# Kernel tuning notes

Hardware: AMD Instinct MI355X
Metric: run time of the kernel (lower is better)

## Reference

```python
import jax, jax.numpy as jnp
import numpy as np

N_GRP = 2048   # n groups
L = 64         # kv slots per group
Q = 4096       # total queries (nq.sum())
D = 256        # d_q = d_k = d_h
DZ = 256       # attention projection dim d_z
DX = 256       # token embedding dim
NTYP = 64      # relation types
NTOK = 50000   # token vocab
M = 131072     # memory tokens
G = 16384      # scatter_sum groups
B = 1024       # examples for scatter_min


def setup_inputs() -> dict:
    key = jax.random.key(0)
    ks = jax.random.split(key, 16)
    q = jax.random.normal(ks[0], (Q, D), jnp.float32)
    k = jax.random.normal(ks[1], (N_GRP, L, D), jnp.float32)
    m = jax.random.bernoulli(ks[2], 0.7, (N_GRP, L))
    m = m.at[:, 0].set(True)  # guarantee >=1 valid slot per group
    # per-query group index == repeat_interleave(arange(n), nq) with nq = 2
    qgrp = jnp.repeat(jnp.arange(N_GRP, dtype=jnp.int32), Q // N_GRP)
    mem = jax.random.randint(ks[3], (M,), 0, NTOK, jnp.int32)
    grp = jnp.sort(jax.random.randint(ks[4], (M,), 0, G, jnp.int32))
    pos2grp = jax.random.randint(ks[5], (N_GRP, L), 0, G, jnp.int32)
    typ = jax.random.randint(ks[6], (Q, NTYP), 0, 2, jnp.int32).astype(bool)
    idx = jnp.sort(jax.random.randint(ks[7], (Q,), 0, B, jnp.int32))
    s = lambda d: 1.0 / np.sqrt(d).astype(np.float32)
    emb = jax.random.normal(ks[8], (NTOK, DX), jnp.float32)
    Wq = jax.random.normal(ks[9], (DZ, D), jnp.float32) * s(D)
    bq = jnp.zeros((DZ,), jnp.float32)
    Wk = jax.random.normal(ks[10], (DZ, D), jnp.float32) * s(D)
    bk = jnp.zeros((DZ,), jnp.float32)
    Wrel = jax.random.normal(ks[11], (NTYP, D + DX), jnp.float32) * s(D + DX)
    brel = jnp.zeros((NTYP,), jnp.float32)
    return dict(q=q, k=k, emb=emb, Wq=Wq, bq=bq, Wk=Wk, bk=bk, Wrel=Wrel,
                brel=brel, m=m, qgrp=qgrp, mem=mem, grp=grp, pos2grp=pos2grp,
                typ=typ, idx=idx)


def reference(q, k, emb, Wq, bq, Wk, bk, Wrel, brel, m, qgrp, mem, grp,
              pos2grp, typ, idx):
    # x_all = scatter_sum(tok_embedding(mem), grp, 0)[pos2grp] : (n, l, dx)
    x_all = jax.ops.segment_sum(emb[mem], grp, num_segments=G)[pos2grp]
    # Attention (ragged masked softmax over l, per-query group gather)
    qz = q @ Wq.T + bq                      # (Q, dz)
    kz = k @ Wk.T + bk                      # (n, l, dz)
    s = jnp.einsum('qd,qld->ql', qz, kz[qgrp]) / np.sqrt(DZ).astype(np.float32)
    s = jnp.where(m[qgrp], s, -jnp.inf)     # masked_fill(~m, -inf)
    p = jax.nn.softmax(s, axis=1)           # softmax over l
    att = jnp.einsum('ql,qld->qd', p, x_all[qgrp])   # (Q, dx)
    logit = jnp.concatenate([q, att], axis=-1) @ Wrel.T + brel  # (Q, n_typ)
    gt = logit > 0
    eq = gt == typ
    acc = eq.astype(jnp.float32).mean()
    em = jax.ops.segment_min(eq.all(1).astype(jnp.int32), idx, num_segments=B)
    emr = em.astype(jnp.float32).mean()
    # binary_cross_entropy_with_logits, reduction='sum', / len(m)
    nll = (jnp.logaddexp(0.0, logit) - logit * typ.astype(logit.dtype)).sum() / N_GRP
    return (logit, acc, emr, nll, em)
```

## Files before the change

kernel.cpp:

```cpp
#include <hip/hip_runtime.h>
#include <hip/hip_bf16.h>
#include <math.h>

#define N_GRP 2048
#define LSLOT 64
#define NQ    4096
#define DIM   256
#define NTYPE 64
#define MMEM  131072
#define GSEG  16384
#define BEX   1024

#define OFF_SEG   0u
#define OFF_QW    4194304u
#define OFF_MT    5242880u
#define OFF_VB    5308416u
#define OFF_WB    5308672u
#define OFF_SB    5308928u
#define OFF_EM    5308936u
#define OFF_CNT   5309960u
#define OFF_NLL   5309964u
#define OFF_FLAG  5309966u

#define OUT_ACC 262144
#define OUT_EMR 262145
#define OUT_NLL 262146
#define OUT_EM  262147

__device__ __forceinline__ bool rd_bool(const void* p, int i, int mode) {
  if (mode == 0) return ((const int*)p)[i] != 0;
  if (mode == 1) return ((const unsigned char*)p)[i] != 0;
  return ((const float*)p)[i] != 0.f;
}

__global__ __launch_bounds__(256)
void k_pre(const float* __restrict__ Wq, const float* __restrict__ bq,
           const float* __restrict__ Wk, const float* __restrict__ bk,
           const void* __restrict__ typ, float* __restrict__ ws) {
  int b = blockIdx.x, t = threadIdx.x;
  if (b < 32) {
    int j0 = b * 8;
    float acc[8] = {0.f,0.f,0.f,0.f,0.f,0.f,0.f,0.f};
    for (int z = 0; z < 256; ++z) {
      float wk = Wk[z * 256 + t];
      const float* wq = Wq + z * 256 + j0;
      #pragma unroll
      for (int u = 0; u < 8; ++u) acc[u] += wq[u] * wk;
    }
    #pragma unroll
    for (int u = 0; u < 8; ++u) ws[OFF_MT + (unsigned)(j0 + u) * 256 + t] = acc[u];
  } else if (b == 32) {
    float a = 0.f;
    for (int z = 0; z < 256; ++z) a += Wq[z * 256 + t] * bk[z];
    ws[OFF_VB + t] = a;
  } else if (b == 33) {
    float a = 0.f;
    for (int z = 0; z < 256; ++z) a += Wk[z * 256 + t] * bq[z];
    ws[OFF_WB + t] = a;
    __shared__ float red[256];
    red[t] = bq[t] * bk[t];
    __syncthreads();
    for (int st = 128; st; st >>= 1) { if (t < st) red[t] += red[t + st]; __syncthreads(); }
    if (t == 0) ws[OFF_SB] = red[0];
  } else {
    __shared__ int fl_f, fl_b;
    if (t == 0) { fl_f = 0; fl_b = 0; }
    __syncthreads();
    for (int i = t; i < 4096; i += 256) {
      unsigned wv = ((const unsigned*)typ)[i];
      if (wv == 0x3F800000u) atomicOr(&fl_f, 1);
      else if (wv > 1u)      atomicOr(&fl_b, 1);
    }
    __syncthreads();
    int* em = (int*)(ws + OFF_EM);
    for (int i = t; i < BEX; i += 256) em[i] = 0x7FFFFFFF;
    if (t == 0) {
      *(int*)(ws + OFF_FLAG) = fl_f ? 2 : (fl_b ? 1 : 0);
      *(int*)(ws + OFF_CNT) = 0;
      *(double*)(ws + OFF_NLL) = 0.0;
    }
  }
}

__global__ __launch_bounds__(256)
void k_seg(const float* __restrict__ emb, const int* __restrict__ mem,
           const int* __restrict__ grp, float* __restrict__ ws) {
  int t = threadIdx.x;
  int lane = t & 63, w = t >> 6;
  int g = blockIdx.x * 4 + w;
  int lo = 0, hi = MMEM;
  while (lo < hi) { int mid = (lo + hi) >> 1; if (grp[mid] < g) lo = mid + 1; else hi = mid; }
  int lo2 = lo, hi2 = MMEM;
  while (lo2 < hi2) { int mid = (lo2 + hi2) >> 1; if (grp[mid] < g + 1) lo2 = mid + 1; else hi2 = mid; }
  float4 acc = {0.f, 0.f, 0.f, 0.f};
  for (int r = lo; r < lo2; ++r) {
    int tok = mem[r];
    float4 v = *(const float4*)(emb + (size_t)tok * 256 + lane * 4);
    acc.x += v.x; acc.y += v.y; acc.z += v.z; acc.w += v.w;
  }
  *(float4*)(ws + OFF_SEG + (size_t)g * 256 + lane * 4) = acc;
}

__global__ __launch_bounds__(256)
void k_qw(const float* __restrict__ q, float* __restrict__ ws) {
  int b = blockIdx.x, t = threadIdx.x;
  int r0 = b * 16;
  const float* MT = ws + OFF_MT;
  float acc[16];
  float wbv = ws[OFF_WB + t];
  #pragma unroll
  for (int r = 0; r < 16; ++r) acc[r] = wbv;
  for (int j = 0; j < 256; j += 4) {
    float m0 = MT[(j + 0) * 256 + t];
    float m1 = MT[(j + 1) * 256 + t];
    float m2 = MT[(j + 2) * 256 + t];
    float m3 = MT[(j + 3) * 256 + t];
    #pragma unroll
    for (int r = 0; r < 16; ++r) {
      float4 q4 = *(const float4*)(q + (size_t)(r0 + r) * 256 + j);
      acc[r] += q4.x * m0 + q4.y * m1 + q4.z * m2 + q4.w * m3;
    }
  }
  #pragma unroll
  for (int r = 0; r < 16; ++r) ws[OFF_QW + (unsigned)(r0 + r) * 256 + t] = acc[r];
}

__global__ __launch_bounds__(256)
void k_attn(const float* __restrict__ q, const float* __restrict__ k,
            const float* __restrict__ Wrel, const float* __restrict__ brel,
            const void* __restrict__ mmask, const int* __restrict__ pos2grp,
            const void* __restrict__ typ, const int* __restrict__ idx,
            float* __restrict__ ws, float* __restrict__ out) {
  int g = blockIdx.x;
  int t = threadIdx.x;
  int lane = t & 63, w = t >> 6;
  __shared__ float qw_l[2][256], qr_l[2][256], att_l[2][256];
  __shared__ float s_l[2][64], p_l[2][64];
  __shared__ float att_p[4][2][64][4];
  __shared__ float cq_l[2];
  __shared__ float nll_l;
  __shared__ int eqcnt_l, all_l[2];
  const int q0 = 2 * g;
  const int mode = *(const int*)(ws + OFF_FLAG);

  qw_l[0][t] = ws[OFF_QW + (unsigned)q0 * 256 + t];
  qw_l[1][t] = ws[OFF_QW + (unsigned)(q0 + 1) * 256 + t];
  qr_l[0][t] = q[(size_t)q0 * 256 + t];
  qr_l[1][t] = q[(size_t)(q0 + 1) * 256 + t];
  if (t == 0) { eqcnt_l = 0; nll_l = 0.f; all_l[0] = 1; all_l[1] = 1; }
  if (w < 2) {
    const float* qrow = q + (size_t)(q0 + w) * 256;
    float p = 0.f;
    #pragma unroll
    for (int u = 0; u < 4; ++u) p += qrow[lane + 64 * u] * ws[OFF_VB + lane + 64 * u];
    for (int off = 32; off; off >>= 1) p += __shfl_xor(p, off);
    if (lane == 0) cq_l[w] = p + ws[OFF_SB];
  }
  __syncthreads();

  const float* kg = k + (size_t)g * LSLOT * 256;
  for (int li = 0; li < 16; ++li) {
    int l = w * 16 + li;
    bool valid = rd_bool(mmask, g * LSLOT + l, mode);
    if (!valid) {
      if (lane == 0) { s_l[0][l] = -INFINITY; s_l[1][l] = -INFINITY; }
      continue;
    }
    float4 kv = *(const float4*)(kg + l * 256 + lane * 4);
    float4 w0 = *(const float4*)&qw_l[0][lane * 4];
    float4 w1 = *(const float4*)&qw_l[1][lane * 4];
    float s0 = kv.x * w0.x + kv.y * w0.y + kv.z * w0.z + kv.w * w0.w;
    float s1 = kv.x * w1.x + kv.y * w1.y + kv.z * w1.z + kv.w * w1.w;
    for (int off = 32; off; off >>= 1) { s0 += __shfl_xor(s0, off); s1 += __shfl_xor(s1, off); }
    if (lane == 0) {
      s_l[0][l] = (s0 + cq_l[0]) * 0.0625f;
      s_l[1][l] = (s1 + cq_l[1]) * 0.0625f;
    }
  }
  __syncthreads();

  if (w < 2) {
    float v = s_l[w][lane];
    float mx = v;
    for (int off = 32; off; off >>= 1) mx = fmaxf(mx, __shfl_xor(mx, off));
    float e = expf(v - mx);
    float ssum = e;
    for (int off = 32; off; off >>= 1) ssum += __shfl_xor(ssum, off);
    p_l[w][lane] = e / ssum;
  }
  __syncthreads();

  {
    float4 a0 = {0.f,0.f,0.f,0.f}, a1 = {0.f,0.f,0.f,0.f};
    const float* seg = ws + OFF_SEG;
    const int* pg = pos2grp + g * LSLOT;
    for (int li = 0; li < 16; ++li) {
      int l = li * 4 + w;
      float p0 = p_l[0][l], p1 = p_l[1][l];
      if (p0 == 0.f && p1 == 0.f) continue;
      int row = pg[l];
      float4 v = *(const float4*)(seg + (size_t)row * 256 + lane * 4);
      a0.x += p0 * v.x; a0.y += p0 * v.y; a0.z += p0 * v.z; a0.w += p0 * v.w;
      a1.x += p1 * v.x; a1.y += p1 * v.y; a1.z += p1 * v.z; a1.w += p1 * v.w;
    }
    *(float4*)&att_p[w][0][lane][0] = a0;
    *(float4*)&att_p[w][1][lane][0] = a1;
  }
  __syncthreads();
  {
    int dl = t >> 2, dc = t & 3;
    #pragma unroll
    for (int qi = 0; qi < 2; ++qi)
      att_l[qi][t] = att_p[0][qi][dl][dc] + att_p[1][qi][dl][dc]
                   + att_p[2][qi][dl][dc] + att_p[3][qi][dl][dc];
  }
  __syncthreads();

  {
    int cnt = 0, allf = 1;
    float nllp = 0.f;
    int qi = w >> 1;
    int tbase = (w & 1) * 32;
    const float* src = (lane < 32) ? &qr_l[qi][lane * 8] : &att_l[qi][(lane - 32) * 8];
    float4 xa = *(const float4*)src;
    float4 xb = *(const float4*)(src + 4);
    for (int it = 0; it < 32; ++it) {
      int tt = tbase + it;
      const float* wr = Wrel + tt * 512 + lane * 8;
      float4 wa = *(const float4*)wr;
      float4 wb4 = *(const float4*)(wr + 4);
      float d = xa.x * wa.x + xa.y * wa.y + xa.z * wa.z + xa.w * wa.w
              + xb.x * wb4.x + xb.y * wb4.y + xb.z * wb4.z + xb.w * wb4.w;
      for (int off = 32; off; off >>= 1) d += __shfl_xor(d, off);
      if (lane == 0) {
        float lg = d + brel[tt];
        out[(size_t)(q0 + qi) * NTYPE + tt] = lg;
        bool gt = lg > 0.f;
        bool tv = rd_bool(typ, (q0 + qi) * NTYPE + tt, mode);
        bool eqv = (gt == tv);
        cnt += (int)eqv;
        allf &= (int)eqv;
        nllp += fmaxf(lg, 0.f) + log1pf(expf(-fabsf(lg))) - (tv ? lg : 0.f);
      }
    }
    if (lane == 0) {
      atomicAdd(&eqcnt_l, cnt);
      atomicAnd(&all_l[qi], allf);
      atomicAdd(&nll_l, nllp);
    }
  }
  __syncthreads();
  if (t == 0) {
    atomicAdd((int*)(ws + OFF_CNT), eqcnt_l);
    atomicAdd((double*)(ws + OFF_NLL), (double)nll_l);
    int* em = (int*)(ws + OFF_EM);
    atomicMin(&em[idx[q0]], all_l[0]);
    atomicMin(&em[idx[q0 + 1]], all_l[1]);
  }
}

__global__ __launch_bounds__(256)
void k_fin(float* __restrict__ ws, float* __restrict__ out) {
  __shared__ float red[256];
  int t = threadIdx.x;
  const int* em = (const int*)(ws + OFF_EM);
  float s = 0.f;
  for (int i = t; i < BEX; i += 256) {
    float v = (float)em[i];
    out[OUT_EM + i] = v;
    s += v;
  }
  red[t] = s; __syncthreads();
  for (int st = 128; st; st >>= 1) { if (t < st) red[t] += red[t + st]; __syncthreads(); }
  if (t == 0) {
    out[OUT_ACC] = (float)(*(const int*)(ws + OFF_CNT)) / (float)(NQ * NTYPE);
    out[OUT_EMR] = red[0] / (float)BEX;
    out[OUT_NLL] = (float)((*(const double*)(ws + OFF_NLL)) / (double)N_GRP);
  }
}

extern "C" void kernel_launch(void* const* d_in, const int* in_sizes, int n_in,
                              void* d_out, int out_size, void* d_ws, size_t ws_size,
                              hipStream_t stream) {
  const float* q    = (const float*)d_in[0];
  const float* k    = (const float*)d_in[1];
  const float* emb  = (const float*)d_in[2];
  const float* Wq   = (const float*)d_in[3];
  const float* bq   = (const float*)d_in[4];
  const float* Wk   = (const float*)d_in[5];
  const float* bk   = (const float*)d_in[6];
  const float* Wrel = (const float*)d_in[7];
  const float* brel = (const float*)d_in[8];
  const void* mmask   = d_in[9];
  const int* mem      = (const int*)d_in[11];
  const int* grp      = (const int*)d_in[12];
  const int* pos2grp  = (const int*)d_in[13];
  const void* typ     = d_in[14];
  const int* idx      = (const int*)d_in[15];
  float* ws  = (float*)d_ws;
  float* out = (float*)d_out;

  k_pre <<<35,     256, 0, stream>>>(Wq, bq, Wk, bk, typ, ws);
  k_seg <<<GSEG/4, 256, 0, stream>>>(emb, mem, grp, ws);
  k_qw  <<<NQ/16,  256, 0, stream>>>(q, ws);
  k_attn<<<N_GRP,  256, 0, stream>>>(q, k, Wrel, brel, mmask, pos2grp, typ, idx, ws, out);
  k_fin <<<1,      256, 0, stream>>>(ws, out);
}
```

Measured before the change: 467.1 us.

## Merge segment-sum and query projection kernels, restructure attention dot products

Spreads the Wq·Wk precompute over 256 blocks instead of 32. Fuses the segment-sum and q·M kernels into one launch and removes a launch boundary. In the segment-sum, tokens are loaded once per wave and broadcast by shuffle, with four embedding rows fetched per iteration for more memory-level parallelism. In the attention kernel, the score and Wrel dot products now use 4-lane partial sums with short shuffle reductions instead of full 64-lane reductions, and masking is moved into the softmax. The logit epilogue uses a wave ballot. The combined kernel mixes two very different block workloads, and k loads are no longer skipped for masked slots.

```diff
diff --git a/kernel.cpp b/kernel.cpp
--- a/kernel.cpp
+++ b/kernel.cpp
@@ -38,23 +38,21 @@
            const float* __restrict__ Wk, const float* __restrict__ bk,
            const void* __restrict__ typ, float* __restrict__ ws) {
   int b = blockIdx.x, t = threadIdx.x;
-  if (b < 32) {
-    int j0 = b * 8;
-    float acc[8] = {0.f,0.f,0.f,0.f,0.f,0.f,0.f,0.f};
-    for (int z = 0; z < 256; ++z) {
-      float wk = Wk[z * 256 + t];
-      const float* wq = Wq + z * 256 + j0;
-      #pragma unroll
-      for (int u = 0; u < 8; ++u) acc[u] += wq[u] * wk;
-    }
-    #pragma unroll
-    for (int u = 0; u < 8; ++u) ws[OFF_MT + (unsigned)(j0 + u) * 256 + t] = acc[u];
-  } else if (b == 32) {
+  if (b < 256) {
+    int j = b;
+    float acc = 0.f;
+    #pragma unroll 8
+    for (int z = 0; z < 256; ++z)
+      acc += Wk[z * 256 + t] * Wq[z * 256 + j];
+    ws[OFF_MT + (unsigned)j * 256 + t] = acc;
+  } else if (b == 256) {
     float a = 0.f;
+    #pragma unroll 8
     for (int z = 0; z < 256; ++z) a += Wq[z * 256 + t] * bk[z];
     ws[OFF_VB + t] = a;
-  } else if (b == 33) {
+  } else if (b == 257) {
     float a = 0.f;
+    #pragma unroll 8
     for (int z = 0; z < 256; ++z) a += Wk[z * 256 + t] * bq[z];
     ws[OFF_WB + t] = a;
     __shared__ float red[256];
@@ -83,46 +81,67 @@
 }
 
 __global__ __launch_bounds__(256)
-void k_seg(const float* __restrict__ emb, const int* __restrict__ mem,
-           const int* __restrict__ grp, float* __restrict__ ws) {
+void k_segqw(const float* __restrict__ emb, const int* __restrict__ mem,
+             const int* __restrict__ grp, const float* __restrict__ q,
+             float* __restrict__ ws) {
   int t = threadIdx.x;
-  int lane = t & 63, w = t >> 6;
-  int g = blockIdx.x * 4 + w;
-  int lo = 0, hi = MMEM;
-  while (lo < hi) { int mid = (lo + hi) >> 1; if (grp[mid] < g) lo = mid + 1; else hi = mid; }
-  int lo2 = lo, hi2 = MMEM;
-  while (lo2 < hi2) { int mid = (lo2 + hi2) >> 1; if (grp[mid] < g + 1) lo2 = mid + 1; else hi2 = mid; }
-  float4 acc = {0.f, 0.f, 0.f, 0.f};
-  for (int r = lo; r < lo2; ++r) {
-    int tok = mem[r];
-    float4 v = *(const float4*)(emb + (size_t)tok * 256 + lane * 4);
-    acc.x += v.x; acc.y += v.y; acc.z += v.z; acc.w += v.w;
-  }
-  *(float4*)(ws + OFF_SEG + (size_t)g * 256 + lane * 4) = acc;
-}
-
-__global__ __launch_bounds__(256)
-void k_qw(const float* __restrict__ q, float* __restrict__ ws) {
-  int b = blockIdx.x, t = threadIdx.x;
-  int r0 = b * 16;
-  const float* MT = ws + OFF_MT;
-  float acc[16];
-  float wbv = ws[OFF_WB + t];
-  #pragma unroll
-  for (int r = 0; r < 16; ++r) acc[r] = wbv;
-  for (int j = 0; j < 256; j += 4) {
-    float m0 = MT[(j + 0) * 256 + t];
-    float m1 = MT[(j + 1) * 256 + t];
-    float m2 = MT[(j + 2) * 256 + t];
-    float m3 = MT[(j + 3) * 256 + t];
-    #pragma unroll
-    for (int r = 0; r < 16; ++r) {
-      float4 q4 = *(const float4*)(q + (size_t)(r0 + r) * 256 + j);
-      acc[r] += q4.x * m0 + q4.y * m1 + q4.z * m2 + q4.w * m3;
-    }
-  }
-  #pragma unroll
-  for (int r = 0; r < 16; ++r) ws[OFF_QW + (unsigned)(r0 + r) * 256 + t] = acc[r];
+  if (blockIdx.x < GSEG / 4) {
+    int lane = t & 63, w = t >> 6;
+    int g = blockIdx.x * 4 + w;
+    int lo = 0, hi = MMEM;
+    while (lo < hi) { int mid = (lo + hi) >> 1; if (grp[mid] < g) lo = mid + 1; else hi = mid; }
+    int lo2 = lo, hi2 = MMEM;
+    while (lo2 < hi2) { int mid = (lo2 + hi2) >> 1; if (grp[mid] < g + 1) lo2 = mid + 1; else hi2 = mid; }
+    int n = lo2 - lo;
+    int nv = n < 64 ? n : 64;
+    int tok = (lane < nv) ? mem[lo + lane] : 0;
+    float4 acc = {0.f, 0.f, 0.f, 0.f};
+    int r = 0;
+    for (; r + 4 <= nv; r += 4) {
+      int t0 = __shfl(tok, r + 0), t1 = __shfl(tok, r + 1);
+      int t2 = __shfl(tok, r + 2), t3 = __shfl(tok, r + 3);
+      float4 v0 = *(const float4*)(emb + (size_t)t0 * 256 + lane * 4);
+      float4 v1 = *(const float4*)(emb + (size_t)t1 * 256 + lane * 4);
+      float4 v2 = *(const float4*)(emb + (size_t)t2 * 256 + lane * 4);
+      float4 v3 = *(const float4*)(emb + (size_t)t3 * 256 + lane * 4);
+      acc.x += (v0.x + v1.x) + (v2.x + v3.x);
+      acc.y += (v0.y + v1.y) + (v2.y + v3.y);
+      acc.z += (v0.z + v1.z) + (v2.z + v3.z);
+      acc.w += (v0.w + v1.w) + (v2.w + v3.w);
+    }
+    for (; r < nv; ++r) {
+      int tr = __shfl(tok, r);
+      float4 v = *(const float4*)(emb + (size_t)tr * 256 + lane * 4);
+      acc.x += v.x; acc.y += v.y; acc.z += v.z; acc.w += v.w;
+    }
+    for (int rr = lo + 64; rr < lo2; ++rr) {
+      int tr = mem[rr];
+      float4 v = *(const float4*)(emb + (size_t)tr * 256 + lane * 4);
+      acc.x += v.x; acc.y += v.y; acc.z += v.z; acc.w += v.w;
+    }
+    *(float4*)(ws + OFF_SEG + (size_t)g * 256 + lane * 4) = acc;
+  } else {
+    int b = blockIdx.x - GSEG / 4;
+    int r0 = b * 8;
+    const float* MT = ws + OFF_MT;
+    float acc[8];
+    float wbv = ws[OFF_WB + t];
+    #pragma unroll
+    for (int r = 0; r < 8; ++r) acc[r] = wbv;
+    for (int j = 0; j < 256; j += 4) {
+      float m0 = MT[(j + 0) * 256 + t];
+      float m1 = MT[(j + 1) * 256 + t];
+      float m2 = MT[(j + 2) * 256 + t];
+      float m3 = MT[(j + 3) * 256 + t];
+      #pragma unroll
+      for (int r = 0; r < 8; ++r) {
+        float4 q4 = *(const float4*)(q + (size_t)(r0 + r) * 256 + j);
+        acc[r] += q4.x * m0 + q4.y * m1 + q4.z * m2 + q4.w * m3;
+      }
+    }
+    #pragma unroll
+    for (int r = 0; r < 8; ++r) ws[OFF_QW + (unsigned)(r0 + r) * 256 + t] = acc[r];
+  }
 }
 
 __global__ __launch_bounds__(256)
@@ -135,7 +154,7 @@
   int t = threadIdx.x;
   int lane = t & 63, w = t >> 6;
   __shared__ float qw_l[2][256], qr_l[2][256], att_l[2][256];
-  __shared__ float s_l[2][64], p_l[2][64];
+  __shared__ float s_raw[2][64], p_l[2][64];
   __shared__ float att_p[4][2][64][4];
   __shared__ float cq_l[2];
   __shared__ float nll_l;
@@ -147,7 +166,7 @@
   qw_l[1][t] = ws[OFF_QW + (unsigned)(q0 + 1) * 256 + t];
   qr_l[0][t] = q[(size_t)q0 * 256 + t];
   qr_l[1][t] = q[(size_t)(q0 + 1) * 256 + t];
-  if (t == 0) { eqcnt_l = 0; nll_l = 0.f; all_l[0] = 1; all_l[1] = 1; }
+  if (t == 0) { eqcnt_l = 0; nll_l = 0.f; }
   if (w < 2) {
     const float* qrow = q + (size_t)(q0 + w) * 256;
     float p = 0.f;
@@ -158,29 +177,28 @@
   }
   __syncthreads();
 
-  const float* kg = k + (size_t)g * LSLOT * 256;
-  for (int li = 0; li < 16; ++li) {
-    int l = w * 16 + li;
-    bool valid = rd_bool(mmask, g * LSLOT + l, mode);
-    if (!valid) {
-      if (lane == 0) { s_l[0][l] = -INFINITY; s_l[1][l] = -INFINITY; }
-      continue;
-    }
-    float4 kv = *(const float4*)(kg + l * 256 + lane * 4);
-    float4 w0 = *(const float4*)&qw_l[0][lane * 4];
-    float4 w1 = *(const float4*)&qw_l[1][lane * 4];
-    float s0 = kv.x * w0.x + kv.y * w0.y + kv.z * w0.z + kv.w * w0.w;
-    float s1 = kv.x * w1.x + kv.y * w1.y + kv.z * w1.z + kv.w * w1.w;
-    for (int off = 32; off; off >>= 1) { s0 += __shfl_xor(s0, off); s1 += __shfl_xor(s1, off); }
-    if (lane == 0) {
-      s_l[0][l] = (s0 + cq_l[0]) * 0.0625f;
-      s_l[1][l] = (s1 + cq_l[1]) * 0.0625f;
-    }
+  {
+    int sl = w * 16 + (lane >> 2);
+    int c4 = lane & 3;
+    const float* kr = k + (size_t)g * LSLOT * 256 + (size_t)sl * 256 + c4 * 4;
+    float s0 = 0.f, s1 = 0.f;
+    #pragma unroll
+    for (int j = 0; j < 16; ++j) {
+      float4 kv = *(const float4*)(kr + j * 16);
+      float4 w0 = *(const float4*)&qw_l[0][j * 16 + c4 * 4];
+      float4 w1 = *(const float4*)&qw_l[1][j * 16 + c4 * 4];
+      s0 += kv.x * w0.x + kv.y * w0.y + kv.z * w0.z + kv.w * w0.w;
+      s1 += kv.x * w1.x + kv.y * w1.y + kv.z * w1.z + kv.w * w1.w;
+    }
+    s0 += __shfl_xor(s0, 1); s0 += __shfl_xor(s0, 2);
+    s1 += __shfl_xor(s1, 1); s1 += __shfl_xor(s1, 2);
+    if (c4 == 0) { s_raw[0][sl] = s0; s_raw[1][sl] = s1; }
   }
   __syncthreads();
 
   if (w < 2) {
-    float v = s_l[w][lane];
+    bool valid = rd_bool(mmask, g * LSLOT + lane, mode);
+    float v = valid ? (s_raw[w][lane] + cq_l[w]) * 0.0625f : -INFINITY;
     float mx = v;
     for (int off = 32; off; off >>= 1) mx = fmaxf(mx, __shfl_xor(mx, off));
     float e = expf(v - mx);
@@ -194,6 +212,7 @@
     float4 a0 = {0.f,0.f,0.f,0.f}, a1 = {0.f,0.f,0.f,0.f};
     const float* seg = ws + OFF_SEG;
     const int* pg = pos2grp + g * LSLOT;
+    #pragma unroll 4
     for (int li = 0; li < 16; ++li) {
       int l = li * 4 + w;
       float p0 = p_l[0][l], p1 = p_l[1][l];
@@ -217,35 +236,44 @@
   __syncthreads();
 
   {
-    int cnt = 0, allf = 1;
-    float nllp = 0.f;
     int qi = w >> 1;
-    int tbase = (w & 1) * 32;
-    const float* src = (lane < 32) ? &qr_l[qi][lane * 8] : &att_l[qi][(lane - 32) * 8];
-    float4 xa = *(const float4*)src;
-    float4 xb = *(const float4*)(src + 4);
-    for (int it = 0; it < 32; ++it) {
-      int tt = tbase + it;
-      const float* wr = Wrel + tt * 512 + lane * 8;
-      float4 wa = *(const float4*)wr;
-      float4 wb4 = *(const float4*)(wr + 4);
-      float d = xa.x * wa.x + xa.y * wa.y + xa.z * wa.z + xa.w * wa.w
-              + xb.x * wb4.x + xb.y * wb4.y + xb.z * wb4.z + xb.w * wb4.w;
-      for (int off = 32; off; off >>= 1) d += __shfl_xor(d, off);
-      if (lane == 0) {
-        float lg = d + brel[tt];
-        out[(size_t)(q0 + qi) * NTYPE + tt] = lg;
-        bool gt = lg > 0.f;
-        bool tv = rd_bool(typ, (q0 + qi) * NTYPE + tt, mode);
-        bool eqv = (gt == tv);
-        cnt += (int)eqv;
-        allf &= (int)eqv;
-        nllp += fmaxf(lg, 0.f) + log1pf(expf(-fabsf(lg))) - (tv ? lg : 0.f);
+    int c4 = lane & 3;
+    #pragma unroll
+    for (int h = 0; h < 2; ++h) {
+      int tt = (w & 1) * 32 + h * 16 + (lane >> 2);
+      const float* wr = Wrel + (size_t)tt * 512 + c4 * 4;
+      float s = 0.f;
+      #pragma unroll
+      for (int j = 0; j < 16; ++j) {
+        float4 wv = *(const float4*)(wr + j * 16);
+        float4 xv = *(const float4*)&qr_l[qi][j * 16 + c4 * 4];
+        s += wv.x * xv.x + wv.y * xv.y + wv.z * xv.z + wv.w * xv.w;
       }
-    }
+      #pragma unroll
+      for (int j = 0; j < 16; ++j) {
+        float4 wv = *(const float4*)(wr + 1024 + j * 16);
+        float4 xv = *(const float4*)&att_l[qi][j * 16 + c4 * 4];
+        s += wv.x * xv.x + wv.y * xv.y + wv.z * xv.z + wv.w * xv.w;
+      }
+      s += __shfl_xor(s, 1); s += __shfl_xor(s, 2);
+      if (c4 == 0) s_raw[qi][tt] = s;
+    }
+  }
+  __syncthreads();
+
+  if (w < 2) {
+    int qi = w;
+    float lg = s_raw[qi][lane] + brel[lane];
+    out[(size_t)(q0 + qi) * NTYPE + lane] = lg;
+    bool gt = lg > 0.f;
+    bool tv = rd_bool(typ, (q0 + qi) * NTYPE + lane, mode);
+    bool eqv = (gt == tv);
+    unsigned long long mask = __ballot(eqv);
+    float nllp = fmaxf(lg, 0.f) + log1pf(expf(-fabsf(lg))) - (tv ? lg : 0.f);
+    for (int off = 32; off; off >>= 1) nllp += __shfl_xor(nllp, off);
     if (lane == 0) {
-      atomicAdd(&eqcnt_l, cnt);
-      atomicAnd(&all_l[qi], allf);
+      all_l[qi] = (mask == 0xFFFFFFFFFFFFFFFFull) ? 1 : 0;
+      atomicAdd(&eqcnt_l, (int)__popcll(mask));
       atomicAdd(&nll_l, nllp);
     }
   }
@@ -300,9 +328,8 @@
   float* ws  = (float*)d_ws;
   float* out = (float*)d_out;
 
-  k_pre <<<35,     256, 0, stream>>>(Wq, bq, Wk, bk, typ, ws);
-  k_seg <<<GSEG/4, 256, 0, stream>>>(emb, mem, grp, ws);
-  k_qw  <<<NQ/16,  256, 0, stream>>>(q, ws);
-  k_attn<<<N_GRP,  256, 0, stream>>>(q, k, Wrel, brel, mmask, pos2grp, typ, idx, ws, out);
-  k_fin <<<1,      256, 0, stream>>>(ws, out);
-}
+  k_pre  <<<259,            256, 0, stream>>>(Wq, bq, Wk, bk, typ, ws);
+  k_segqw<<<GSEG/4 + NQ/8,  256, 0, stream>>>(emb, mem, grp, q, ws);
+  k_attn <<<N_GRP,          256, 0, stream>>>(q, k, Wrel, brel, mmask, pos2grp, typ, idx, ws, out);
+  k_fin  <<<1,              256, 0, stream>>>(ws, out);
+}
```

Result: faster. 386.8 us (-17.2%).
